# Performance work log

Measured on AMD Instinct MI355X. Metric: run time of the kernel, lower is better.

## Reference

```python
import jax, jax.numpy as jnp
import numpy as np

EPS = 1e-8


def setup_inputs() -> dict:
    key = jax.random.key(0)
    k1, k2, k3 = jax.random.split(key, 3)
    T, B, d, n = 1024, 8, 64, 64
    v = jax.random.normal(k1, (T, B, d), dtype=jnp.float32)
    k = jax.random.normal(k2, (T, B, n), dtype=jnp.float32)
    alpha = jax.random.uniform(k3, (T, B, n), dtype=jnp.float32)
    return {"v": v, "k": k, "alpha": alpha}


def reference(v, k, alpha):
    # v: (T,B,d), k: (T,B,n), alpha: (T,B,n) in [0,1] -> S: (T,B,d,n)
    outer = jnp.einsum('tbd,tbn->tbdn', v, k)          # (T,B,d,n)
    log_alpha = jnp.log(jnp.maximum(alpha, EPS))       # clamp_min(1e-8)
    cumprod = jnp.exp(jnp.cumsum(log_alpha, axis=0))   # (T,B,n)
    decay = cumprod / (cumprod[-1:] + EPS)             # normalize by last step
    weighted = outer * decay[:, :, None, :]            # (T,B,d,n)
    S = jnp.cumsum(weighted, axis=0)
    return S
```

## Files before the change

### kernel.cpp

```cpp
#include <hip/hip_runtime.h>

#define T_DIM 1024
#define B_DIM 8
#define D_DIM 64
#define N_DIM 64

typedef float v4f __attribute__((ext_vector_type(4)));

#define C_CHUNKS 64
#define C_LEN 16
#define SLAB (B_DIM * D_DIM * N_DIM)

#define WS_PSUM 0
#define WS_PXS (C_CHUNKS * SLAB)
#define WS_LSUM (2 * C_CHUNKS * SLAB)

__global__ __launch_bounds__(64) void lsum_kernel(
    const float* __restrict__ alpha, float* __restrict__ lsum) {
  const int b = blockIdx.x >> 6;
  const int c = blockIdx.x & 63;
  const int n = threadIdx.x;

  float s = 0.f;
#pragma unroll
  for (int i = 0; i < C_LEN; ++i) {
    const int t = c * C_LEN + i;
    s += __logf(fmaxf(alpha[((size_t)t * B_DIM + b) * N_DIM + n], 1e-8f));
  }
  lsum[((size_t)b * C_CHUNKS + c) * N_DIM + n] = s;
}

__device__ __forceinline__ void stage_w_v(
    int b, int c, int dt, int tid,
    const float* __restrict__ v, const float* __restrict__ alpha,
    const float* __restrict__ kk, const float* __restrict__ lsum,
    float (*w_t)[N_DIM], float (*v_t)[16]) {
  {
    const int i = tid >> 4;
    const int dl = tid & 15;
    v_t[i][dl] =
        v[((size_t)(c * C_LEN + i) * B_DIM + b) * D_DIM + dt * 16 + dl];
  }
  if (tid < 64) {
    const int n = tid;
    const float* __restrict__ lp = lsum + (size_t)b * C_CHUNKS * N_DIM + n;
    float pre = 0.f, tot = 0.f;
#pragma unroll
    for (int j = 0; j < C_CHUNKS; ++j) {
      const float sj = lp[(size_t)j * N_DIM];
      tot += sj;
      pre += (j < c) ? sj : 0.f;
    }
    const float invden = 1.0f / (__expf(tot) + 1e-8f);
    float cum = pre;
#pragma unroll
    for (int i = 0; i < C_LEN; ++i) {
      const size_t idx = ((size_t)(c * C_LEN + i) * B_DIM + b) * N_DIM + n;
      cum += __logf(fmaxf(alpha[idx], 1e-8f));
      w_t[i][n] = kk[idx] * __expf(cum) * invden;
    }
  }
}

__global__ __launch_bounds__(256) void psum_kernel(
    const float* __restrict__ v, const float* __restrict__ alpha,
    const float* __restrict__ kk, float* __restrict__ ws) {
  __shared__ float w_t[C_LEN][N_DIM];
  __shared__ float v_t[C_LEN][16];
  const int bid = blockIdx.x;
  const int dt = bid & 3;
  const int b  = (bid >> 2) & 7;
  const int c  = bid >> 5;
  const int tid = threadIdx.x;

  stage_w_v(b, c, dt, tid, v, alpha, kk, ws + WS_LSUM, w_t, v_t);
  __syncthreads();

  const int dl = tid >> 4;
  const int n0 = (tid & 15) * 4;
  v4f acc = {0.f, 0.f, 0.f, 0.f};
#pragma unroll
  for (int i = 0; i < C_LEN; ++i) {
    const float vv = v_t[i][dl];
    const v4f w4 = *(const v4f*)&w_t[i][n0];
    acc.x = fmaf(vv, w4.x, acc.x);
    acc.y = fmaf(vv, w4.y, acc.y);
    acc.z = fmaf(vv, w4.z, acc.z);
    acc.w = fmaf(vv, w4.w, acc.w);
  }
  *(v4f*)(ws + WS_PSUM +
          (((size_t)c * B_DIM + b) * D_DIM + dt * 16 + dl) * N_DIM + n0) = acc;
}

__global__ __launch_bounds__(256) void prefix_kernel(float* __restrict__ ws) {
  const int q = blockIdx.x * 256 + threadIdx.x;
  v4f* __restrict__ ps  = (v4f*)(ws + WS_PSUM);
  v4f* __restrict__ pxs = (v4f*)(ws + WS_PXS);

  v4f run = {0.f, 0.f, 0.f, 0.f};
#pragma unroll 8
  for (int c = 0; c < C_CHUNKS; ++c) {
    const v4f p = ps[(size_t)c * (SLAB / 4) + q];
    pxs[(size_t)c * (SLAB / 4) + q] = run;
    run.x += p.x; run.y += p.y; run.z += p.z; run.w += p.w;
  }
}

__global__ __launch_bounds__(256) void scan_store_kernel(
    const float* __restrict__ v, const float* __restrict__ alpha,
    const float* __restrict__ kk, const float* __restrict__ ws,
    float* __restrict__ out) {
  __shared__ float w_t[C_LEN][N_DIM];
  __shared__ float v_t[C_LEN][16];
  const int bid = blockIdx.x;
  const int dt = bid & 3;
  const int b  = (bid >> 2) & 7;
  const int c  = bid >> 5;
  const int tid = threadIdx.x;

  const int dl = tid >> 4;
  const int n0 = (tid & 15) * 4;
  const int d  = dt * 16 + dl;

  v4f acc = *(const v4f*)(ws + WS_PXS +
                          (((size_t)c * B_DIM + b) * D_DIM + d) * N_DIM + n0);

  stage_w_v(b, c, dt, tid, v, alpha, kk, ws + WS_LSUM, w_t, v_t);
  __syncthreads();

#pragma unroll
  for (int i = 0; i < C_LEN; ++i) {
    const int t = c * C_LEN + i;
    const float vv = v_t[i][dl];
    const v4f w4 = *(const v4f*)&w_t[i][n0];
    acc.x = fmaf(vv, w4.x, acc.x);
    acc.y = fmaf(vv, w4.y, acc.y);
    acc.z = fmaf(vv, w4.z, acc.z);
    acc.w = fmaf(vv, w4.w, acc.w);
    *(v4f*)(out + (((size_t)t * B_DIM + b) * D_DIM + d) * N_DIM + n0) = acc;
  }
}

extern "C" void kernel_launch(void* const* d_in, const int* in_sizes, int n_in,
                              void* d_out, int out_size, void* d_ws, size_t ws_size,
                              hipStream_t stream) {
  const float* v     = (const float*)d_in[0];
  const float* k     = (const float*)d_in[1];
  const float* alpha = (const float*)d_in[2];
  float* out = (float*)d_out;
  float* ws  = (float*)d_ws;

  lsum_kernel<<<B_DIM * C_CHUNKS, 64, 0, stream>>>(alpha, ws + WS_LSUM);
  psum_kernel<<<C_CHUNKS * B_DIM * 4, 256, 0, stream>>>(v, alpha, k, ws);
  prefix_kernel<<<SLAB / 4 / 256, 256, 0, stream>>>(ws);
  scan_store_kernel<<<C_CHUNKS * B_DIM * 4, 256, 0, stream>>>(v, alpha, k, ws, out);
}
```

Measured before the change: 163.4 us.

## Fuse chunk-sum, prefix and scan-store into persistent kernel with grid barrier

Replaces the psum, prefix and scan_store kernels with one persistent kernel. Each block computes its chunk partial sums, waits at a hierarchical atomic grid barrier, then sums the preceding chunks' partials directly before writing outputs. Staged tiles stay in shared memory across the barrier when every task has its own block. This removes the separate prefix kernel and its workspace array and avoids restaging tiles. In exchange it adds O(c) partial-sum reads per block, a memset, a device attribute query on each launch, and relies on all blocks being co-resident for the spin barrier.

Result: slower. 460.6 us (+181.8%).

```diff
diff --git a/kernel.cpp b/kernel.cpp
--- a/kernel.cpp
+++ b/kernel.cpp
@@ -9,135 +9,180 @@
 
 #define C_CHUNKS 64
 #define C_LEN 16
+#define NTASK (C_CHUNKS * B_DIM * 4)
 #define SLAB (B_DIM * D_DIM * N_DIM)
 
 #define WS_PSUM 0
-#define WS_PXS (C_CHUNKS * SLAB)
-#define WS_LSUM (2 * C_CHUNKS * SLAB)
-
-__global__ __launch_bounds__(64) void lsum_kernel(
+#define WS_LSUM (C_CHUNKS * SLAB)
+#define WS_BAR (WS_LSUM + B_DIM * C_CHUNKS * N_DIM)
+#define BAR_UINTS (64 * 32 + 2)
+
+__global__ __launch_bounds__(256) void lsum_kernel(
     const float* __restrict__ alpha, float* __restrict__ lsum) {
+  __shared__ float qs[4][N_DIM];
   const int b = blockIdx.x >> 6;
   const int c = blockIdx.x & 63;
-  const int n = threadIdx.x;
+  const int tid = threadIdx.x;
+  const int q = tid >> 6, n = tid & 63;
 
   float s = 0.f;
 #pragma unroll
-  for (int i = 0; i < C_LEN; ++i) {
-    const int t = c * C_LEN + i;
+  for (int i = 0; i < 4; ++i) {
+    const int t = c * C_LEN + q * 4 + i;
     s += __logf(fmaxf(alpha[((size_t)t * B_DIM + b) * N_DIM + n], 1e-8f));
   }
-  lsum[((size_t)b * C_CHUNKS + c) * N_DIM + n] = s;
-}
-
-__device__ __forceinline__ void stage_w_v(
-    int b, int c, int dt, int tid,
+  qs[q][n] = s;
+  __syncthreads();
+  if (tid < 64) {
+    lsum[((size_t)b * C_CHUNKS + c) * N_DIM + tid] =
+        (qs[0][tid] + qs[1][tid]) + (qs[2][tid] + qs[3][tid]);
+  }
+}
+
+__device__ __forceinline__ void grid_barrier(unsigned* bar, unsigned nblk) {
+  __syncthreads();
+  if (threadIdx.x == 0) {
+    __threadfence();
+    unsigned* groups = bar;
+    unsigned* root = bar + 64 * 32;
+    unsigned* gen = root + 1;
+    const unsigned g =
+        __hip_atomic_load(gen, __ATOMIC_RELAXED, __HIP_MEMORY_SCOPE_AGENT);
+    const unsigned gid = blockIdx.x & 63;
+    const unsigned gtarget = ((nblk - 1 - gid) >> 6) + 1;
+    const unsigned ngroups = (nblk < 64) ? nblk : 64;
+    const unsigned a = __hip_atomic_fetch_add(
+        groups + gid * 32, 1u, __ATOMIC_ACQ_REL, __HIP_MEMORY_SCOPE_AGENT);
+    if (a + 1 == gtarget) {
+      __hip_atomic_store(groups + gid * 32, 0u, __ATOMIC_RELAXED,
+                         __HIP_MEMORY_SCOPE_AGENT);
+      const unsigned r = __hip_atomic_fetch_add(
+          root, 1u, __ATOMIC_ACQ_REL, __HIP_MEMORY_SCOPE_AGENT);
+      if (r + 1 == ngroups) {
+        __hip_atomic_store(root, 0u, __ATOMIC_RELAXED, __HIP_MEMORY_SCOPE_AGENT);
+        __hip_atomic_store(gen, g + 1u, __ATOMIC_RELEASE,
+                           __HIP_MEMORY_SCOPE_AGENT);
+      }
+    }
+    while (__hip_atomic_load(gen, __ATOMIC_ACQUIRE, __HIP_MEMORY_SCOPE_AGENT) ==
+           g) {
+      __builtin_amdgcn_s_sleep(4);
+    }
+    __threadfence();
+  }
+  __syncthreads();
+}
+
+__device__ __forceinline__ void stage_tiles(
+    int b, int c, int dt, int tid, const float* __restrict__ v,
+    const float* __restrict__ alpha, const float* __restrict__ kk,
+    const float* __restrict__ lsum, float (*w_t)[N_DIM], float (*v_t)[16],
+    float (*qs)[N_DIM]) {
+  const int q = tid >> 6;
+  const int n = tid & 63;
+
+  const float* __restrict__ lp = lsum + (size_t)b * C_CHUNKS * N_DIM + n;
+  float pre = 0.f, tot = 0.f;
+#pragma unroll 8
+  for (int j = 0; j < C_CHUNKS; ++j) {
+    const float sj = lp[(size_t)j * N_DIM];
+    tot += sj;
+    pre += (j < c) ? sj : 0.f;
+  }
+  const float invden = 1.0f / (__expf(tot) + 1e-8f);
+
+  float la[4];
+  float qsum = 0.f;
+#pragma unroll
+  for (int i = 0; i < 4; ++i) {
+    const int t = c * C_LEN + q * 4 + i;
+    la[i] = __logf(fmaxf(alpha[((size_t)t * B_DIM + b) * N_DIM + n], 1e-8f));
+    qsum += la[i];
+  }
+  qs[q][n] = qsum;
+
+  {
+    const int vi = tid >> 4, dl = tid & 15;
+    v_t[vi][dl] =
+        v[((size_t)(c * C_LEN + vi) * B_DIM + b) * D_DIM + dt * 16 + dl];
+  }
+  __syncthreads();
+
+  float cum = pre;
+#pragma unroll
+  for (int q2 = 0; q2 < 3; ++q2)
+    if (q2 < q) cum += qs[q2][n];
+#pragma unroll
+  for (int i = 0; i < 4; ++i) {
+    const int t = c * C_LEN + q * 4 + i;
+    cum += la[i];
+    w_t[q * 4 + i][n] =
+        kk[((size_t)t * B_DIM + b) * N_DIM + n] * __expf(cum) * invden;
+  }
+  __syncthreads();
+}
+
+__global__ __launch_bounds__(256, 8) void mega_kernel(
     const float* __restrict__ v, const float* __restrict__ alpha,
-    const float* __restrict__ kk, const float* __restrict__ lsum,
-    float (*w_t)[N_DIM], float (*v_t)[16]) {
-  {
-    const int i = tid >> 4;
-    const int dl = tid & 15;
-    v_t[i][dl] =
-        v[((size_t)(c * C_LEN + i) * B_DIM + b) * D_DIM + dt * 16 + dl];
-  }
-  if (tid < 64) {
-    const int n = tid;
-    const float* __restrict__ lp = lsum + (size_t)b * C_CHUNKS * N_DIM + n;
-    float pre = 0.f, tot = 0.f;
-#pragma unroll
-    for (int j = 0; j < C_CHUNKS; ++j) {
-      const float sj = lp[(size_t)j * N_DIM];
-      tot += sj;
-      pre += (j < c) ? sj : 0.f;
-    }
-    const float invden = 1.0f / (__expf(tot) + 1e-8f);
-    float cum = pre;
-#pragma unroll
-    for (int i = 0; i < C_LEN; ++i) {
-      const size_t idx = ((size_t)(c * C_LEN + i) * B_DIM + b) * N_DIM + n;
-      cum += __logf(fmaxf(alpha[idx], 1e-8f));
-      w_t[i][n] = kk[idx] * __expf(cum) * invden;
-    }
-  }
-}
-
-__global__ __launch_bounds__(256) void psum_kernel(
-    const float* __restrict__ v, const float* __restrict__ alpha,
-    const float* __restrict__ kk, float* __restrict__ ws) {
-  __shared__ float w_t[C_LEN][N_DIM];
-  __shared__ float v_t[C_LEN][16];
-  const int bid = blockIdx.x;
-  const int dt = bid & 3;
-  const int b  = (bid >> 2) & 7;
-  const int c  = bid >> 5;
-  const int tid = threadIdx.x;
-
-  stage_w_v(b, c, dt, tid, v, alpha, kk, ws + WS_LSUM, w_t, v_t);
-  __syncthreads();
-
-  const int dl = tid >> 4;
-  const int n0 = (tid & 15) * 4;
-  v4f acc = {0.f, 0.f, 0.f, 0.f};
-#pragma unroll
-  for (int i = 0; i < C_LEN; ++i) {
-    const float vv = v_t[i][dl];
-    const v4f w4 = *(const v4f*)&w_t[i][n0];
-    acc.x = fmaf(vv, w4.x, acc.x);
-    acc.y = fmaf(vv, w4.y, acc.y);
-    acc.z = fmaf(vv, w4.z, acc.z);
-    acc.w = fmaf(vv, w4.w, acc.w);
-  }
-  *(v4f*)(ws + WS_PSUM +
-          (((size_t)c * B_DIM + b) * D_DIM + dt * 16 + dl) * N_DIM + n0) = acc;
-}
-
-__global__ __launch_bounds__(256) void prefix_kernel(float* __restrict__ ws) {
-  const int q = blockIdx.x * 256 + threadIdx.x;
-  v4f* __restrict__ ps  = (v4f*)(ws + WS_PSUM);
-  v4f* __restrict__ pxs = (v4f*)(ws + WS_PXS);
-
-  v4f run = {0.f, 0.f, 0.f, 0.f};
-#pragma unroll 8
-  for (int c = 0; c < C_CHUNKS; ++c) {
-    const v4f p = ps[(size_t)c * (SLAB / 4) + q];
-    pxs[(size_t)c * (SLAB / 4) + q] = run;
-    run.x += p.x; run.y += p.y; run.z += p.z; run.w += p.w;
-  }
-}
-
-__global__ __launch_bounds__(256) void scan_store_kernel(
-    const float* __restrict__ v, const float* __restrict__ alpha,
-    const float* __restrict__ kk, const float* __restrict__ ws,
+    const float* __restrict__ kk, float* __restrict__ ws,
     float* __restrict__ out) {
   __shared__ float w_t[C_LEN][N_DIM];
   __shared__ float v_t[C_LEN][16];
-  const int bid = blockIdx.x;
-  const int dt = bid & 3;
-  const int b  = (bid >> 2) & 7;
-  const int c  = bid >> 5;
+  __shared__ float qs[4][N_DIM];
+
   const int tid = threadIdx.x;
-
+  const unsigned nblk = gridDim.x;
+  const float* lsum = ws + WS_LSUM;
+  unsigned* bar = (unsigned*)(ws + WS_BAR);
   const int dl = tid >> 4;
   const int n0 = (tid & 15) * 4;
-  const int d  = dt * 16 + dl;
-
-  v4f acc = *(const v4f*)(ws + WS_PXS +
-                          (((size_t)c * B_DIM + b) * D_DIM + d) * N_DIM + n0);
-
-  stage_w_v(b, c, dt, tid, v, alpha, kk, ws + WS_LSUM, w_t, v_t);
-  __syncthreads();
-
-#pragma unroll
-  for (int i = 0; i < C_LEN; ++i) {
-    const int t = c * C_LEN + i;
-    const float vv = v_t[i][dl];
-    const v4f w4 = *(const v4f*)&w_t[i][n0];
-    acc.x = fmaf(vv, w4.x, acc.x);
-    acc.y = fmaf(vv, w4.y, acc.y);
-    acc.z = fmaf(vv, w4.z, acc.z);
-    acc.w = fmaf(vv, w4.w, acc.w);
-    *(v4f*)(out + (((size_t)t * B_DIM + b) * D_DIM + d) * N_DIM + n0) = acc;
+
+  for (unsigned task = blockIdx.x; task < NTASK; task += nblk) {
+    const int dt = task & 3, b = (task >> 2) & 7, c = task >> 5;
+    stage_tiles(b, c, dt, tid, v, alpha, kk, lsum, w_t, v_t, qs);
+    v4f acc = {0.f, 0.f, 0.f, 0.f};
+#pragma unroll
+    for (int i = 0; i < C_LEN; ++i) {
+      const float vv = v_t[i][dl];
+      const v4f w4 = *(const v4f*)&w_t[i][n0];
+      acc.x = fmaf(vv, w4.x, acc.x);
+      acc.y = fmaf(vv, w4.y, acc.y);
+      acc.z = fmaf(vv, w4.z, acc.z);
+      acc.w = fmaf(vv, w4.w, acc.w);
+    }
+    *(v4f*)(ws + WS_PSUM +
+            (((size_t)c * B_DIM + b) * D_DIM + dt * 16 + dl) * N_DIM + n0) = acc;
+    __syncthreads();
+  }
+
+  grid_barrier(bar, nblk);
+
+  const bool tiles_live = (nblk >= NTASK);
+  for (unsigned task = blockIdx.x; task < NTASK; task += nblk) {
+    const int dt = task & 3, b = (task >> 2) & 7, c = task >> 5;
+    if (!tiles_live) stage_tiles(b, c, dt, tid, v, alpha, kk, lsum, w_t, v_t, qs);
+    const int d = dt * 16 + dl;
+
+    v4f acc = {0.f, 0.f, 0.f, 0.f};
+    const float* __restrict__ pp =
+        ws + WS_PSUM + ((size_t)b * D_DIM + d) * N_DIM + n0;
+#pragma unroll 4
+    for (int j = 0; j < c; ++j) {
+      const v4f p = *(const v4f*)(pp + (size_t)j * SLAB);
+      acc.x += p.x; acc.y += p.y; acc.z += p.z; acc.w += p.w;
+    }
+#pragma unroll
+    for (int i = 0; i < C_LEN; ++i) {
+      const int t = c * C_LEN + i;
+      const float vv = v_t[i][dl];
+      const v4f w4 = *(const v4f*)&w_t[i][n0];
+      acc.x = fmaf(vv, w4.x, acc.x);
+      acc.y = fmaf(vv, w4.y, acc.y);
+      acc.z = fmaf(vv, w4.z, acc.z);
+      acc.w = fmaf(vv, w4.w, acc.w);
+      *(v4f*)(out + (((size_t)t * B_DIM + b) * D_DIM + d) * N_DIM + n0) = acc;
+    }
+    __syncthreads();
   }
 }
 
@@ -150,8 +195,20 @@
   float* out = (float*)d_out;
   float* ws  = (float*)d_ws;
 
-  lsum_kernel<<<B_DIM * C_CHUNKS, 64, 0, stream>>>(alpha, ws + WS_LSUM);
-  psum_kernel<<<C_CHUNKS * B_DIM * 4, 256, 0, stream>>>(v, alpha, k, ws);
-  prefix_kernel<<<SLAB / 4 / 256, 256, 0, stream>>>(ws);
-  scan_store_kernel<<<C_CHUNKS * B_DIM * 4, 256, 0, stream>>>(v, alpha, k, ws, out);
-}
+  int dev = 0, cus = 0;
+  if (hipGetDevice(&dev) != hipSuccess) dev = 0;
+  if (hipDeviceGetAttribute(&cus, hipDeviceAttributeMultiprocessorCount, dev) !=
+          hipSuccess ||
+      cus <= 0) {
+    cus = 256;
+  }
+  unsigned nblk = (unsigned)cus * 8u;
+  if (nblk > NTASK) nblk = NTASK;
+  if (nblk == 0) nblk = 1;
+
+  (void)hipMemsetAsync((void*)(ws + WS_BAR), 0, BAR_UINTS * sizeof(unsigned),
+                       stream);
+
+  lsum_kernel<<<B_DIM * C_CHUNKS, 256, 0, stream>>>(alpha, ws + WS_LSUM);
+  mega_kernel<<<nblk, 256, 0, stream>>>(v, alpha, k, ws, out);
+}
```
